# Kernel optimization log

Hardware: AMD Instinct MI355X
Metric: run time of the kernel (lower is better)

The kernel has to match this reference:

```python
import jax, jax.numpy as jnp
import numpy as np

STRIDES = [8, 16, 32, 64, 128]
SIZES = [32.0, 64.0, 128.0, 256.0, 512.0]
FEAT_HW = [(100, 152), (50, 76), (25, 38), (13, 19), (7, 10)]
N, C, A, K = 2, 256, 9, 80
SCORE_TH, TOPK, NMS_TH, MAX_DET = 0.05, 1000, 0.5, 100
IMG_H, IMG_W = 800.0, 1216.0
SCALE_CLAMP = float(np.log(1000.0 / 16.0))


def _cell_anchors(size):
    ratios = [0.5, 1.0, 2.0]
    scales = [2 ** 0, 2 ** (1.0 / 3), 2 ** (2.0 / 3)]
    out = []
    for s in scales:
        area = (size * s) ** 2
        for r in ratios:
            w = np.sqrt(area / r)
            h = w * r
            out.append([-w / 2.0, -h / 2.0, w / 2.0, h / 2.0])
    return np.asarray(out, np.float32)  # (9, 4)


def make_anchors():
    ancs = []
    for (H, W), st, sz in zip(FEAT_HW, STRIDES, SIZES):
        cell = _cell_anchors(sz)
        sx = np.arange(W, dtype=np.float32) * st
        sy = np.arange(H, dtype=np.float32) * st
        gx, gy = np.meshgrid(sx, sy)
        shifts = np.stack([gx.ravel(), gy.ravel(), gx.ravel(), gy.ravel()], 1)
        ancs.append((shifts[:, None, :] + cell[None, :, :]).reshape(-1, 4).astype(np.float32))
    return ancs


def setup_inputs() -> dict:
    key = jax.random.key(0)
    ks = jax.random.split(key, 10)
    inp = {}
    for i, (H, W) in enumerate(FEAT_HW):
        inp[f"feat{i}"] = jax.random.normal(ks[i], (N, C, H, W), jnp.float32)
    inp["cls_sub_w"] = jax.random.normal(ks[5], (4, C, C, 3, 3), jnp.float32) * 0.01
    inp["cls_sub_b"] = jnp.zeros((4, C), jnp.float32)
    inp["bbox_sub_w"] = jax.random.normal(ks[6], (4, C, C, 3, 3), jnp.float32) * 0.01
    inp["bbox_sub_b"] = jnp.zeros((4, C), jnp.float32)
    inp["cls_score_w"] = jax.random.normal(ks[7], (A * K, C, 3, 3), jnp.float32) * 0.1
    inp["cls_score_b"] = jnp.full((A * K,), float(-np.log((1 - 0.01) / 0.01)), jnp.float32)
    inp["bbox_pred_w"] = jax.random.normal(ks[8], (A * 4, C, 3, 3), jnp.float32) * 0.01
    inp["bbox_pred_b"] = jnp.zeros((A * 4,), jnp.float32)
    for i, a in enumerate(make_anchors()):
        inp[f"anc{i}"] = jnp.asarray(a)
    return inp


def conv3(x, w, b):
    y = jax.lax.conv_general_dilated(x, w, (1, 1), 'SAME',
                                     dimension_numbers=('NCHW', 'OIHW', 'NCHW'))
    return y + b[None, :, None, None]


def head_level(x, csw, csb, bsw, bsb, scw, scb, bpw, bpb):
    c = x
    r = x
    for i in range(4):
        c = jax.nn.relu(conv3(c, csw[i], csb[i]))
        r = jax.nn.relu(conv3(r, bsw[i], bsb[i]))
    return conv3(c, scw, scb), conv3(r, bpw, bpb)


def to_NHWA_K(t, k):
    n, _, h, w = t.shape
    return t.reshape(n, -1, k, h, w).transpose(0, 3, 4, 1, 2).reshape(n, -1, k)


def decode(deltas, anchors):
    wa = anchors[..., 2] - anchors[..., 0]
    ha = anchors[..., 3] - anchors[..., 1]
    xa = anchors[..., 0] + 0.5 * wa
    ya = anchors[..., 1] + 0.5 * ha
    dx, dy = deltas[..., 0], deltas[..., 1]
    dw = jnp.minimum(deltas[..., 2], SCALE_CLAMP)
    dh = jnp.minimum(deltas[..., 3], SCALE_CLAMP)
    cx = dx * wa + xa
    cy = dy * ha + ya
    w = jnp.exp(dw) * wa
    h = jnp.exp(dh) * ha
    return jnp.stack([cx - 0.5 * w, cy - 0.5 * h, cx + 0.5 * w, cy + 0.5 * h], -1)


def iou_vs_all(box, boxes):
    lt = jnp.maximum(box[:2], boxes[:, :2])
    rb = jnp.minimum(box[2:], boxes[:, 2:])
    wh = jnp.clip(rb - lt, 0.0)
    inter = wh[:, 0] * wh[:, 1]
    a1 = (box[2] - box[0]) * (box[3] - box[1])
    a2 = (boxes[:, 2] - boxes[:, 0]) * (boxes[:, 3] - boxes[:, 1])
    return inter / (a1 + a2 - inter + 1e-9)


def nms_image(boxes, scores, classes):
    # class-aware NMS via coordinate offset per class (batched_nms trick)
    off = classes.astype(boxes.dtype)[:, None] * 4096.0
    b = boxes + off

    def body(i, st):
        sc, bi, bs = st
        j = jnp.argmax(sc)
        s = sc[j]
        bi = bi.at[i].set(j)
        bs = bs.at[i].set(s)
        iou = iou_vs_all(b[j], b)
        sc = jnp.where(iou > NMS_TH, 0.0, sc).at[j].set(0.0)
        return (sc, bi, bs)

    bi0 = jnp.zeros((MAX_DET,), jnp.int32)
    bs0 = jnp.zeros((MAX_DET,), boxes.dtype)
    _, bi, bs = jax.lax.fori_loop(0, MAX_DET, body, (scores, bi0, bs0))
    return boxes[bi], bs, classes[bi]


def reference(feat0, feat1, feat2, feat3, feat4, cls_sub_w, cls_sub_b,
              bbox_sub_w, bbox_sub_b, cls_score_w, cls_score_b,
              bbox_pred_w, bbox_pred_b, anc0, anc1, anc2, anc3, anc4):
    feats = [feat0, feat1, feat2, feat3, feat4]
    ancs = [anc0, anc1, anc2, anc3, anc4]
    cand_b, cand_s, cand_c = [], [], []
    for f, anc in zip(feats, ancs):
        logits, deltas = head_level(f, cls_sub_w, cls_sub_b, bbox_sub_w, bbox_sub_b,
                                    cls_score_w, cls_score_b, bbox_pred_w, bbox_pred_b)
        cls = to_NHWA_K(logits, K)       # (N, HWA, K)
        reg = to_NHWA_K(deltas, 4)       # (N, HWA, 4)
        n, hwa, _ = reg.shape
        prob = jax.nn.sigmoid(cls.reshape(n, hwa * K))
        ntk = min(TOPK, hwa)             # d2: min(topk_candidates, box_reg_i.size(0))
        vals, idxs = jax.lax.top_k(prob, ntk)
        a_idx = idxs // K
        c_idx = idxs % K
        d = jnp.take_along_axis(reg, a_idx[..., None], axis=1)   # (N, ntk, 4)
        anc_sel = anc[a_idx]                                      # (N, ntk, 4)
        boxes = decode(d, anc_sel)
        boxes = jnp.stack([jnp.clip(boxes[..., 0], 0.0, IMG_W),
                           jnp.clip(boxes[..., 1], 0.0, IMG_H),
                           jnp.clip(boxes[..., 2], 0.0, IMG_W),
                           jnp.clip(boxes[..., 3], 0.0, IMG_H)], -1)
        scores = jnp.where(vals > SCORE_TH, vals, 0.0)  # score threshold (keep_idxs)
        cand_b.append(boxes)
        cand_s.append(scores)
        cand_c.append(c_idx)
    B = jnp.concatenate(cand_b, 1)
    S = jnp.concatenate(cand_s, 1)
    Cl = jnp.concatenate(cand_c, 1)
    det_boxes, det_scores, det_classes = jax.vmap(nms_image)(B, S, Cl)
    return det_boxes, det_scores, det_classes
```

## Files before the change

kernel.cpp:

```cpp
#include <hip/hip_runtime.h>
#include <math.h>

#define NIMG 2
#define NCAND 4630
#define MAXDET 100
#define IMG_W_F 1216.0f
#define IMG_H_F 800.0f
#define SCORE_THR 0.05f
#define NMS_THR 0.5f
#define SCALE_CLAMP_F 4.135166556742356f

typedef __attribute__((ext_vector_type(8))) _Float16 f16x8;
typedef __attribute__((ext_vector_type(16))) float f32x16;

#define WOFF_CLS_T(i) ((unsigned)(i) * 589824u)
#define WOFF_BBX_T(i) (2359296u + (unsigned)(i) * 589824u)
#define WOFF_CLS_H 4718592u
#define WOFF_BBX_H 6488064u

#define BUF_HALFS 10944000u
#define TK_SLOT_U32 139272

struct ConvTab {
  int cum[6];
  int H[5], W[5];
  unsigned actOff[5];
};
struct CvtTab {
  const float* f[5];
  int cumR[6];
  int H[5], W[5];
  unsigned actOff[5];
};
struct HeadTab {
  int cum[6];
  unsigned actOff[5];
  int H[5], W[5];
  int pOffL[5];
  int rOffL[5];
  int imgBase;
  int pImgStride;
};
struct TKTab {
  int pOff[9]; int M[9]; int kk[9]; int rBase[9]; int outBase[9];
  const float* anc[9];
};
struct PPTab {
  const float* src[10];
  unsigned dstOff[10];
  int Cout[10];
  int nCoF[10];
  int cum[11];
};

__global__ __launch_bounds__(256)
void prepack_k(_Float16* __restrict__ dst0, PPTab tb)
{
  int t0 = blockIdx.x * 256 + threadIdx.x;
  if (t0 >= tb.cum[10]) return;
  int r = 0;
  for (int i = 1; i < 10; ++i) if (t0 >= tb.cum[i]) r = i;
  const int t = t0 - tb.cum[r];
  const float* src = tb.src[r];
  _Float16* dst = dst0 + tb.dstOff[r];
  const int Cout = tb.Cout[r], nCoF = tb.nCoF[r];

  const int l = t & 63;
  const int rest = t >> 6;
  const int coF = rest % nCoF;
  const int tc = rest / nCoF;
  const int tap = tc >> 4;
  const int cb = tc & 15;
  const int co = coF * 32 + (l & 31);
  const int ciB = cb * 16 + (l >> 5) * 8;
#pragma unroll
  for (int j = 0; j < 8; ++j) {
    float v = 0.f;
    if (co < Cout) v = src[(size_t)(co * 256 + ciB + j) * 9 + tap];
    dst[(size_t)t * 8 + j] = (_Float16)v;
  }
}

__global__ __launch_bounds__(256)
void convert_k(_Float16* __restrict__ act, CvtTab tb)
{
  int bz = blockIdx.x;
  int l = 0;
#pragma unroll
  for (int i = 1; i < 5; ++i) if (bz >= tb.cumR[i]) l = i;
  const int h = bz - tb.cumR[l];
  const int n = blockIdx.y;
  const int H = tb.H[l], W = tb.W[l];
  const int Hp = H + 2, Wp = W + 2, HpWp = Hp * Wp;
  const unsigned CBS = 2u * (unsigned)HpWp * 16u;
  const float* x = tb.f[l];
  _Float16* a = act + tb.actOff[l];
  __shared__ float s[64][154];
  for (int c0 = 0; c0 < 256; c0 += 64) {
    for (int idx = threadIdx.x; idx < 64 * W; idx += 256) {
      int c = idx / W, w = idx - c * W;
      s[c][w] = x[((size_t)(n * 256 + c0 + c) * H + h) * W + w];
    }
    __syncthreads();
    for (int idx = threadIdx.x; idx < 4 * W; idx += 256) {
      int ch = idx / W, w = idx - ch * W;
      int cchunk = (c0 >> 4) + ch;
      unsigned base = (unsigned)cchunk * CBS +
                      ((unsigned)((n * Hp + h + 1) * Wp + (w + 1))) * 16u;
      f16x8 v0, v1;
#pragma unroll
      for (int j = 0; j < 8; ++j) {
        v0[j] = (_Float16)s[ch * 16 + j][w];
        v1[j] = (_Float16)s[ch * 16 + 8 + j][w];
      }
      *(f16x8*)(a + base) = v0;
      *(f16x8*)(a + base + 8) = v1;
    }
    __syncthreads();
  }
}

__device__ __forceinline__ void conv_core(
    const _Float16* __restrict__ in, const _Float16* __restrict__ w,
    int nCoF, int coF0, int Wp, unsigned CBS, const unsigned V0, const unsigned V1,
    unsigned lOff, f32x16& a00, f32x16& a01, f32x16& a10, f32x16& a11)
{
  for (int cb = 0; cb < 16; ++cb) {
    const _Float16* aB = in + (unsigned)cb * CBS;
    const _Float16* wB = w + ((unsigned)cb * (unsigned)nCoF + (unsigned)coF0) * 512u;
#pragma unroll
    for (int tap = 0; tap < 9; ++tap) {
      const unsigned to = ((unsigned)((tap / 3) * Wp + (tap % 3))) * 16u;
      const _Float16* wT = wB + (unsigned)tap * 16u * (unsigned)nCoF * 512u;
      f16x8 a0 = *(const f16x8*)(aB + to + V0);
      f16x8 a1 = *(const f16x8*)(aB + to + V1);
      f16x8 b0 = *(const f16x8*)(wT + lOff);
      f16x8 b1 = *(const f16x8*)(wT + 512u + lOff);
      a00 = __builtin_amdgcn_mfma_f32_32x32x16_f16(a0, b0, a00, 0, 0, 0);
      a01 = __builtin_amdgcn_mfma_f32_32x32x16_f16(a0, b1, a01, 0, 0, 0);
      a10 = __builtin_amdgcn_mfma_f32_32x32x16_f16(a1, b0, a10, 0, 0, 0);
      a11 = __builtin_amdgcn_mfma_f32_32x32x16_f16(a1, b1, a11, 0, 0, 0);
    }
  }
}

__global__ __launch_bounds__(256)
void tower_k(const _Float16* __restrict__ inA, const _Float16* __restrict__ inB,
             const _Float16* __restrict__ wpk,
             const float* __restrict__ biasA, const float* __restrict__ biasB,
             _Float16* __restrict__ outA, _Float16* __restrict__ outB,
             unsigned wOffA, unsigned wOffB, ConvTab tb)
{
  int bz = blockIdx.x;
  int l = 0;
#pragma unroll
  for (int i = 1; i < 5; ++i) if (bz >= tb.cum[i]) l = i;
  const int bx = bz - tb.cum[l];
  const int H = tb.H[l], W = tb.W[l];
  const int Wp = W + 2, HW = H * W, HpWp = (H + 2) * Wp;
  const unsigned CBS = 2u * (unsigned)HpWp * 16u;
  const int chain = blockIdx.y >> 2, cg = blockIdx.y & 3;
  const _Float16* in = (chain ? inB : inA) + tb.actOff[l];
  _Float16* out = (chain ? outB : outA) + tb.actOff[l];
  const _Float16* w = wpk + (chain ? wOffB : wOffA);
  const float* bias = chain ? biasB : biasA;
  const int Mloc = 2 * HW;

  const int wave = threadIdx.x >> 6;
  const int lane = threadIdx.x & 63;
  const int lw = lane & 31;
  const int lh = lane >> 5;
  const int mBase = bx * 256 + wave * 64;
  unsigned V[2];
#pragma unroll
  for (int i = 0; i < 2; ++i) {
    int mloc = mBase + i * 32 + lw;
    if (mloc >= Mloc) mloc = Mloc - 1;
    int n = mloc / HW; int rem = mloc - n * HW;
    int h = rem / W; int ww = rem - h * W;
    V[i] = ((unsigned)(n * HpWp + h * Wp + ww)) * 16u + (unsigned)lh * 8u;
  }
  f32x16 a00 = {}, a01 = {}, a10 = {}, a11 = {};
  conv_core(in, w, 8, cg * 2, Wp, CBS, V[0], V[1], (unsigned)lane * 8u,
            a00, a01, a10, a11);

  const int coBase = cg * 64;
  const f32x16* accs[4] = {&a00, &a01, &a10, &a11};
#pragma unroll
  for (int q = 0; q < 4; ++q) {
    const f32x16& A = *accs[q];
    const int i = q >> 1, f = q & 1;
    const int co = coBase + f * 32 + lw;
    const float bv = bias[co];
#pragma unroll
    for (int r = 0; r < 16; ++r) {
      int mloc = mBase + i * 32 + ((r & 3) + 8 * (r >> 2) + 4 * lh);
      if (mloc >= Mloc) continue;
      int n = mloc / HW; int rem = mloc - n * HW;
      int h = rem / W; int ww = rem - h * W;
      unsigned addr = ((unsigned)(co >> 4)) * CBS +
                      ((unsigned)(n * HpWp + (h + 1) * Wp + (ww + 1))) * 16u +
                      (unsigned)(co & 15);
      out[addr] = (_Float16)fmaxf(A[r] + bv, 0.f);
    }
  }
}

__global__ __launch_bounds__(256)
void head_k(const _Float16* __restrict__ inC, const _Float16* __restrict__ inX,
            const _Float16* __restrict__ wpk,
            const float* __restrict__ scb, const float* __restrict__ bpb,
            float* __restrict__ P, _Float16* __restrict__ Rh, HeadTab tb)
{
  int bz = blockIdx.y;
  int li = 0;
#pragma unroll
  for (int i = 1; i < 5; ++i) if (bz >= tb.cum[i]) li = i;
  const int bx = bz - tb.cum[li];
  const int H = tb.H[li], W = tb.W[li];
  const int Wp = W + 2, HW = H * W, HpWp = (H + 2) * Wp;
  const unsigned CBS = 2u * (unsigned)HpWp * 16u;
  const int img = tb.imgBase + blockIdx.z;
  const int y = blockIdx.x;

  const _Float16* in;
  const _Float16* w;
  const float* bias;
  int nCoF, coF0, coBase, Cout;
  if (y < 12) {
    in = inC + tb.actOff[li]; w = wpk + WOFF_CLS_H; bias = scb;
    nCoF = 24; coF0 = y * 2; coBase = y * 64; Cout = 720;
  } else {
    in = inX + tb.actOff[li]; w = wpk + WOFF_BBX_H; bias = bpb;
    nCoF = 2; coF0 = 0; coBase = 0; Cout = 36;
  }
  const int Mloc = HW;
  const int wave = threadIdx.x >> 6;
  const int lane = threadIdx.x & 63;
  const int lw = lane & 31;
  const int lh = lane >> 5;
  const int mBase = bx * 256 + wave * 64;
  unsigned V[2];
#pragma unroll
  for (int i = 0; i < 2; ++i) {
    int mloc = mBase + i * 32 + lw;
    if (mloc >= Mloc) mloc = Mloc - 1;
    int h = mloc / W; int ww = mloc - h * W;
    V[i] = ((unsigned)(img * HpWp + h * Wp + ww)) * 16u + (unsigned)lh * 8u;
  }
  f32x16 a00 = {}, a01 = {}, a10 = {}, a11 = {};
  conv_core(in, w, nCoF, coF0, Wp, CBS, V[0], V[1], (unsigned)lane * 8u,
            a00, a01, a10, a11);

  const size_t pBase = (size_t)tb.pOffL[li] + (size_t)blockIdx.z * tb.pImgStride;
  const size_t rBase = (size_t)tb.rOffL[li] + (size_t)img * HW * 36;
  const f32x16* accs[4] = {&a00, &a01, &a10, &a11};
#pragma unroll
  for (int q = 0; q < 4; ++q) {
    const f32x16& A = *accs[q];
    const int i = q >> 1, f = q & 1;
    const int co = coBase + f * 32 + lw;
    const float bv = (co < Cout) ? bias[co] : 0.f;
#pragma unroll
    for (int r = 0; r < 16; ++r) {
      int mloc = mBase + i * 32 + ((r & 3) + 8 * (r >> 2) + 4 * lh);
      if (mloc >= Mloc) continue;
      float v = A[r] + bv;
      if (y < 12) {
        if (co < 720) P[pBase + (size_t)mloc * 720 + co] = 1.f / (1.f + expf(-v));
      } else {
        if (co < 36) Rh[rBase + (size_t)mloc * 36 + co] = (_Float16)v;
      }
    }
  }
}

__global__ __launch_bounds__(256)
void hist_coarse_k(const float* __restrict__ wsF, unsigned* __restrict__ tkbuf, TKTab t)
{
  const int slot = blockIdx.y;
  __shared__ unsigned lh[8192];
  for (int i = threadIdx.x; i < 8192; i += 256) lh[i] = 0;
  __syncthreads();
  const float* p = wsF + t.pOff[slot];
  const int M = t.M[slot];
  for (int i = blockIdx.x * 256 + threadIdx.x; i < M; i += gridDim.x * 256)
    atomicAdd(&lh[(__float_as_uint(p[i]) >> 17) & 8191u], 1u);
  __syncthreads();
  unsigned* h = tkbuf + (size_t)slot * TK_SLOT_U32;
  for (int i = threadIdx.x; i < 8192; i += 256) {
    unsigned c = lh[i];
    if (c) atomicAdd(&h[i], c);
  }
}

__global__ __launch_bounds__(256)
void hist_fine_k(const float* __restrict__ wsF, unsigned* __restrict__ tkbuf, TKTab t)
{
  const int slot = blockIdx.y;
  unsigned* base = tkbuf + (size_t)slot * TK_SLOT_U32;
  const unsigned cb = base[8192 + 131072 + 0];
  const float* p = wsF + t.pOff[slot];
  const int M = t.M[slot];
  unsigned* h = base + 8192;
  for (int i = blockIdx.x * 256 + threadIdx.x; i < M; i += gridDim.x * 256) {
    unsigned b = __float_as_uint(p[i]);
    if ((b >> 17) == cb) atomicAdd(&h[b & 0x1FFFFu], 1u);
  }
}

__global__ __launch_bounds__(1024)
void radix_scan_k(unsigned* __restrict__ tkbuf, TKTab t, int phase)
{
  const int slot = blockIdx.x;
  unsigned* base = tkbuf + (size_t)slot * TK_SLOT_U32;
  const unsigned* hb0 = base + (phase ? 8192 : 0);
  unsigned* s = base + 8192 + 131072;
  const int nbins = phase ? 131072 : 8192;
  const int k = t.kk[slot];
  const int per = nbins / 1024;
  const int tid = threadIdx.x;
  const unsigned* hb = hb0 + tid * per;
  unsigned local = 0;
  for (int i = 0; i < per; ++i) local += hb[i];
  __shared__ unsigned part[1024];
  part[tid] = local;
  __syncthreads();
  for (int d = 1; d < 1024; d <<= 1) {
    unsigned v = (tid + d < 1024) ? part[tid + d] : 0u;
    __syncthreads();
    part[tid] += v;
    __syncthreads();
  }
  unsigned above = part[tid] - local;
  unsigned kk = (phase == 0) ? (unsigned)k : ((unsigned)k - s[1]);
  if (above < kk && above + local >= kk) {
    unsigned cum = above;
    for (int i = per - 1; i >= 0; --i) {
      unsigned c = hb[i];
      if (cum + c >= kk) {
        if (phase == 0) { s[0] = (unsigned)(tid * per + i); s[1] = cum; }
        else { s[2] = (s[0] << 17) | (unsigned)(tid * per + i); s[4] = kk - cum; }
        break;
      }
      cum += c;
    }
  }
}

__global__ __launch_bounds__(256)
void compact_k(const float* __restrict__ wsF, unsigned* __restrict__ tkbuf,
               float* __restrict__ cv, unsigned* __restrict__ ci,
               unsigned* __restrict__ eq, TKTab t)
{
  const int slot = blockIdx.y;
  unsigned* s = tkbuf + (size_t)slot * TK_SLOT_U32 + 8192 + 131072;
  const unsigned thr = s[2];
  const float* p = wsF + t.pOff[slot];
  const int M = t.M[slot];
  float* cvn = cv + slot * 1024;
  unsigned* cin_ = ci + slot * 1024;
  unsigned* eqn = eq + (size_t)slot * 8192;
  for (int i = blockIdx.x * 256 + threadIdx.x; i < M; i += gridDim.x * 256) {
    unsigned b = __float_as_uint(p[i]);
    if (b > thr) {
      unsigned g = atomicAdd(&s[5], 1u);
      if (g < 1024u) { cvn[g] = p[i]; cin_[g] = (unsigned)i; }
    } else if (b == thr) {
      unsigned e = atomicAdd(&s[6], 1u);
      if (e < 8192u) eqn[e] = (unsigned)i;
    }
  }
}

__global__ __launch_bounds__(1024)
void finalize_k(const float* __restrict__ cv, const unsigned* __restrict__ ci,
                const unsigned* __restrict__ eq, const unsigned* __restrict__ tkbuf,
                const _Float16* __restrict__ Rh, TKTab t,
                float* __restrict__ candB, float* __restrict__ candS, float* __restrict__ candC)
{
  const int slot = blockIdx.x;
  const int tid = threadIdx.x;
  const unsigned* s = tkbuf + (size_t)slot * TK_SLOT_U32 + 8192 + 131072;
  const float* anc = t.anc[slot];
  const int k = t.kk[slot];
  __shared__ float svals[1024];
  __shared__ unsigned sidx[1024];
  __shared__ unsigned long long key[1024];
  const unsigned cntG = s[5] < 1024u ? s[5] : 1024u;
  const unsigned nEq = s[4];
  if (tid < (int)cntG) {
    svals[tid] = cv[slot * 1024 + tid];
    sidx[tid] = ci[slot * 1024 + tid];
  }
  __syncthreads();
  if (tid == 0) {
    unsigned cnt = s[6] < 8192u ? s[6] : 8192u;
    unsigned last = 0; int first = 1;
    float tv = __uint_as_float(s[2]);
    for (unsigned e2 = 0; e2 < nEq && cntG + e2 < 1024u; ++e2) {
      unsigned best = 0xFFFFFFFFu;
      for (unsigned q = 0; q < cnt; ++q) {
        unsigned v = eq[(size_t)slot * 8192 + q];
        if ((first || v > last) && v < best) best = v;
      }
      svals[cntG + e2] = tv; sidx[cntG + e2] = best;
      last = best; first = 0;
    }
  }
  __syncthreads();
  const int kk = (int)cntG + (int)nEq;
  key[tid] = (tid < kk)
      ? (((unsigned long long)__float_as_uint(svals[tid]) << 32) |
         (unsigned long long)(0xFFFFFFFFu - sidx[tid]))
      : 0ULL;
  __syncthreads();
  for (int sz = 2; sz <= 1024; sz <<= 1) {
    for (int st = sz >> 1; st > 0; st >>= 1) {
      int ixj = tid ^ st;
      if (ixj > tid) {
        unsigned long long a = key[tid], b = key[ixj];
        bool up = ((tid & sz) == 0);
        if (up ? (a < b) : (a > b)) { key[tid] = b; key[ixj] = a; }
      }
      __syncthreads();
    }
  }
  if (tid < kk && tid < k) {
    unsigned long long kv = key[tid];
    float val = __uint_as_float((unsigned)(kv >> 32));
    unsigned idx = 0xFFFFFFFFu - (unsigned)(kv & 0xFFFFFFFFu);
    unsigned a = idx / 80u;
    unsigned cls = idx - a * 80u;
    const _Float16* rg = Rh + (size_t)t.rBase[slot] + (size_t)a * 4;
    float a0 = anc[(size_t)a * 4 + 0], a1 = anc[(size_t)a * 4 + 1];
    float a2 = anc[(size_t)a * 4 + 2], a3 = anc[(size_t)a * 4 + 3];
    float wa = a2 - a0, ha = a3 - a1;
    float xa = a0 + 0.5f * wa, ya = a1 + 0.5f * ha;
    float dx = (float)rg[0], dy = (float)rg[1];
    float dw = fminf((float)rg[2], SCALE_CLAMP_F), dh = fminf((float)rg[3], SCALE_CLAMP_F);
    float cx = dx * wa + xa, cy = dy * ha + ya;
    float wb = expf(dw) * wa, hb = expf(dh) * ha;
    float x0 = cx - 0.5f * wb, y0 = cy - 0.5f * hb;
    float x1 = cx + 0.5f * wb, y1 = cy + 0.5f * hb;
    x0 = fminf(fmaxf(x0, 0.f), IMG_W_F);
    y0 = fminf(fmaxf(y0, 0.f), IMG_H_F);
    x1 = fminf(fmaxf(x1, 0.f), IMG_W_F);
    y1 = fminf(fmaxf(y1, 0.f), IMG_H_F);
    int o = t.outBase[slot] + tid;
    candB[(size_t)o * 4 + 0] = x0; candB[(size_t)o * 4 + 1] = y0;
    candB[(size_t)o * 4 + 2] = x1; candB[(size_t)o * 4 + 3] = y1;
    candS[o] = (val > SCORE_THR) ? val : 0.f;
    candC[o] = (float)cls;
  }
}

__global__ __launch_bounds__(1024)
void nms_k(const float* __restrict__ cB, const float* __restrict__ cS,
           const float* __restrict__ cC, float* __restrict__ out)
{
  const int n = blockIdx.x;
  const int tid = threadIdx.x;
  const int wid = tid >> 6, lane = tid & 63;
  __shared__ float S[NCAND];
  __shared__ float wv_[16];
  __shared__ int wi_[16];
  __shared__ float bj[5];
  __shared__ int sjs;
  for (int i = tid; i < NCAND; i += 1024) S[i] = cS[n * NCAND + i];
  __syncthreads();
  for (int it = 0; it < MAXDET; ++it) {
    float bv = -1.f; int bix = 0;
    for (int i = tid; i < NCAND; i += 1024) {
      float v = S[i];
      if (v > bv) { bv = v; bix = i; }
    }
#pragma unroll
    for (int d = 32; d > 0; d >>= 1) {
      float v2 = __shfl_down(bv, d);
      int i2 = __shfl_down(bix, d);
      if (v2 > bv || (v2 == bv && i2 < bix)) { bv = v2; bix = i2; }
    }
    if (lane == 0) { wv_[wid] = bv; wi_[wid] = bix; }
    __syncthreads();
    if (tid < 64) {
      float v = (tid < 16) ? wv_[tid] : -2.f;
      int ix = (tid < 16) ? wi_[tid] : 0x7FFFFFFF;
#pragma unroll
      for (int d = 8; d > 0; d >>= 1) {
        float v2 = __shfl_down(v, d);
        int i2 = __shfl_down(ix, d);
        if (v2 > v || (v2 == v && i2 < ix)) { v = v2; ix = i2; }
      }
      if (tid == 0) {
        bj[4] = v; sjs = ix;
        if (v > 0.f) {
          const int j = ix;
          float b0 = cB[(size_t)(n * NCAND + j) * 4 + 0];
          float b1 = cB[(size_t)(n * NCAND + j) * 4 + 1];
          float b2 = cB[(size_t)(n * NCAND + j) * 4 + 2];
          float b3 = cB[(size_t)(n * NCAND + j) * 4 + 3];
          out[((size_t)n * MAXDET + it) * 4 + 0] = b0;
          out[((size_t)n * MAXDET + it) * 4 + 1] = b1;
          out[((size_t)n * MAXDET + it) * 4 + 2] = b2;
          out[((size_t)n * MAXDET + it) * 4 + 3] = b3;
          out[800 + n * MAXDET + it] = v;
          out[1000 + n * MAXDET + it] = cC[n * NCAND + j];
          float off = cC[n * NCAND + j] * 4096.f;
          bj[0] = b0 + off; bj[1] = b1 + off; bj[2] = b2 + off; bj[3] = b3 + off;
        }
      }
    }
    __syncthreads();
    const float mv = bj[4];
    const int j = sjs;
    if (mv <= 0.f) {
      float b0 = cB[(size_t)(n * NCAND) * 4 + 0], b1 = cB[(size_t)(n * NCAND) * 4 + 1];
      float b2 = cB[(size_t)(n * NCAND) * 4 + 2], b3 = cB[(size_t)(n * NCAND) * 4 + 3];
      float c0 = cC[n * NCAND];
      for (int t2 = it + tid; t2 < MAXDET; t2 += 1024) {
        out[((size_t)n * MAXDET + t2) * 4 + 0] = b0;
        out[((size_t)n * MAXDET + t2) * 4 + 1] = b1;
        out[((size_t)n * MAXDET + t2) * 4 + 2] = b2;
        out[((size_t)n * MAXDET + t2) * 4 + 3] = b3;
        out[800 + n * MAXDET + t2] = 0.f;
        out[1000 + n * MAXDET + t2] = c0;
      }
      return;
    }
    const float jx0 = bj[0], jy0 = bj[1], jx1 = bj[2], jy1 = bj[3];
    const float aj = (jx1 - jx0) * (jy1 - jy0);
    for (int i = tid; i < NCAND; i += 1024) {
      if (i == j) { S[i] = 0.f; continue; }
      if (S[i] == 0.f) continue;
      float off = cC[n * NCAND + i] * 4096.f;
      float x0 = cB[(size_t)(n * NCAND + i) * 4 + 0] + off;
      float y0 = cB[(size_t)(n * NCAND + i) * 4 + 1] + off;
      float x1 = cB[(size_t)(n * NCAND + i) * 4 + 2] + off;
      float y1 = cB[(size_t)(n * NCAND + i) * 4 + 3] + off;
      float lx = fmaxf(jx0, x0), ly = fmaxf(jy0, y0);
      float rx = fminf(jx1, x1), ry = fminf(jy1, y1);
      float iw = fmaxf(rx - lx, 0.f), ih = fmaxf(ry - ly, 0.f);
      float inter = iw * ih;
      float ai = (x1 - x0) * (y1 - y0);
      float iou = inter / (aj + ai - inter + 1e-9f);
      if (iou > NMS_THR) S[i] = 0.f;
    }
    __syncthreads();
  }
}

extern "C" void kernel_launch(void* const* d_in, const int* in_sizes, int n_in,
                              void* d_out, int out_size, void* d_ws, size_t ws_size,
                              hipStream_t stream)
{
  static const int LH[5] = {100, 50, 25, 13, 7};
  static const int LW[5] = {152, 76, 38, 19, 10};
  static const int LHW[5] = {15200, 3800, 950, 247, 70};
  static const int NTK[5] = {1000, 1000, 1000, 1000, 630};
  static const int OFFS[5] = {0, 1000, 2000, 3000, 4000};
  static const unsigned ACTOFF[5] = {0u, 8042496u, 10119168u, 10672128u, 10833408u};
  static const int CUMT[6] = {0, 119, 149, 157, 159, 160};
  static const int CUMR[6] = {0, 100, 150, 175, 188, 195};
  static const int ROFF[5] = {0, 1094400, 1368000, 1436400, 1454184};
  static const int POFF14[4] = {0, 2736000, 3420000, 3597840};
  static const int PSTRIDE14 = 3648240;

  const float* feat[5]; const float* anc[5];
  for (int l = 0; l < 5; ++l) {
    feat[l] = (const float*)d_in[l];
    anc[l] = (const float*)d_in[13 + l];
  }
  const float* csw = (const float*)d_in[5];
  const float* csb = (const float*)d_in[6];
  const float* bsw = (const float*)d_in[7];
  const float* bsb = (const float*)d_in[8];
  const float* scw = (const float*)d_in[9];
  const float* scb = (const float*)d_in[10];
  const float* bpw = (const float*)d_in[11];
  const float* bpb = (const float*)d_in[12];

  float* wsF = (float*)d_ws;
  size_t o = 0;
  _Float16* actBase = (_Float16*)(wsF + o); o += (size_t)4 * BUF_HALFS / 2;
  _Float16* wpk = (_Float16*)(wsF + o); o += 3317760;
  float* P0 = wsF + o; o += 10944000;
  _Float16* Rh = (_Float16*)(wsF + o); o += 729612;
  float* candB = wsF + o; o += (size_t)NIMG * NCAND * 4;
  float* candS = wsF + o; o += NIMG * NCAND;
  float* candC = wsF + o; o += NIMG * NCAND;
  float* candV = wsF + o; o += 9 * 1024;
  unsigned* candI = (unsigned*)(wsF + o); o += 9 * 1024;
  unsigned* eqI = (unsigned*)(wsF + o); o += 9 * 8192;
  unsigned* tkbuf = (unsigned*)(wsF + o); o += (size_t)9 * TK_SLOT_U32;
  if (ws_size < o * sizeof(float)) return;

  _Float16* X = actBase;
  _Float16* A = X + BUF_HALFS;
  _Float16* B = A + BUF_HALFS;
  _Float16* C = B + BUF_HALFS;
  float* P1 = (float*)A;
  float* out = (float*)d_out;

  {
    PPTab pp;
    static const int PPC[11] = {0, 73728, 147456, 221184, 294912, 368640,
                                442368, 516096, 589824, 811008, 829440};
    for (int i = 0; i < 11; ++i) pp.cum[i] = PPC[i];
    for (int i = 0; i < 4; ++i) {
      pp.src[i] = csw + (size_t)i * 589824; pp.dstOff[i] = WOFF_CLS_T(i);
      pp.Cout[i] = 256; pp.nCoF[i] = 8;
      pp.src[4 + i] = bsw + (size_t)i * 589824; pp.dstOff[4 + i] = WOFF_BBX_T(i);
      pp.Cout[4 + i] = 256; pp.nCoF[4 + i] = 8;
    }
    pp.src[8] = scw; pp.dstOff[8] = WOFF_CLS_H; pp.Cout[8] = 720; pp.nCoF[8] = 24;
    pp.src[9] = bpw; pp.dstOff[9] = WOFF_BBX_H; pp.Cout[9] = 36; pp.nCoF[9] = 2;
    prepack_k<<<dim3(3240), dim3(256), 0, stream>>>(wpk, pp);
  }

  hipMemsetAsync(actBase, 0, (size_t)4 * BUF_HALFS * 2, stream);

  ConvTab ct;
  CvtTab vt;
  for (int l = 0; l < 5; ++l) {
    ct.H[l] = LH[l]; ct.W[l] = LW[l]; ct.actOff[l] = ACTOFF[l];
    vt.f[l] = feat[l]; vt.H[l] = LH[l]; vt.W[l] = LW[l]; vt.actOff[l] = ACTOFF[l];
  }
  for (int i = 0; i < 6; ++i) { ct.cum[i] = CUMT[i]; vt.cumR[i] = CUMR[i]; }

  convert_k<<<dim3(195, NIMG), dim3(256), 0, stream>>>(X, vt);

  tower_k<<<dim3(160, 8), dim3(256), 0, stream>>>(X, X, wpk, csb + 0, bsb + 0, A, B,
      WOFF_CLS_T(0), WOFF_BBX_T(0), ct);
  tower_k<<<dim3(160, 8), dim3(256), 0, stream>>>(A, B, wpk, csb + 256, bsb + 256, C, X,
      WOFF_CLS_T(1), WOFF_BBX_T(1), ct);
  tower_k<<<dim3(160, 8), dim3(256), 0, stream>>>(C, X, wpk, csb + 512, bsb + 512, A, B,
      WOFF_CLS_T(2), WOFF_BBX_T(2), ct);
  tower_k<<<dim3(160, 8), dim3(256), 0, stream>>>(A, B, wpk, csb + 768, bsb + 768, C, X,
      WOFF_CLS_T(3), WOFF_BBX_T(3), ct);

  auto runTopk = [&](const TKTab& tk, int nslot) {
    hipMemsetAsync(tkbuf, 0, (size_t)nslot * TK_SLOT_U32 * 4, stream);
    hist_coarse_k<<<dim3(256, nslot), dim3(256), 0, stream>>>(wsF, tkbuf, tk);
    radix_scan_k<<<dim3(nslot), dim3(1024), 0, stream>>>(tkbuf, tk, 0);
    hist_fine_k<<<dim3(256, nslot), dim3(256), 0, stream>>>(wsF, tkbuf, tk);
    radix_scan_k<<<dim3(nslot), dim3(1024), 0, stream>>>(tkbuf, tk, 1);
    compact_k<<<dim3(256, nslot), dim3(256), 0, stream>>>(wsF, tkbuf, candV, candI, eqI, tk);
    finalize_k<<<dim3(nslot), dim3(1024), 0, stream>>>(candV, candI, eqI, tkbuf, Rh, tk,
                                                       candB, candS, candC);
  };

  const int p0Off = (int)(P0 - wsF);
  const int p1Off = (int)(P1 - wsF);

  {
    HeadTab ht = {};
    ht.cum[0] = 0; ht.cum[1] = 60;
    for (int i = 2; i < 6; ++i) ht.cum[i] = 0x7FFFFFFF;
    ht.actOff[0] = ACTOFF[0]; ht.H[0] = LH[0]; ht.W[0] = LW[0];
    ht.pOffL[0] = 0; ht.rOffL[0] = ROFF[0];
    ht.imgBase = 0; ht.pImgStride = 0;
    head_k<<<dim3(13, 60, 1), dim3(256), 0, stream>>>(C, X, wpk, scb, bpb, P0, Rh, ht);
    TKTab tk = {};
    tk.pOff[0] = p0Off; tk.M[0] = LHW[0] * 720; tk.kk[0] = NTK[0];
    tk.rBase[0] = ROFF[0];
    tk.outBase[0] = OFFS[0];
    tk.anc[0] = anc[0];
    runTopk(tk, 1);
  }
  {
    HeadTab ht = {};
    ht.cum[0] = 0; ht.cum[1] = 60;
    for (int i = 2; i < 6; ++i) ht.cum[i] = 0x7FFFFFFF;
    ht.actOff[0] = ACTOFF[0]; ht.H[0] = LH[0]; ht.W[0] = LW[0];
    ht.pOffL[0] = 0; ht.rOffL[0] = ROFF[0];
    ht.imgBase = 1; ht.pImgStride = 0;
    head_k<<<dim3(13, 60, 1), dim3(256), 0, stream>>>(C, X, wpk, scb, bpb, P1, Rh, ht);
  }
  {
    HeadTab ht = {};
    static const int CUMH14[6] = {0, 15, 19, 20, 21, 0x7FFFFFFF};
    for (int i = 0; i < 6; ++i) ht.cum[i] = CUMH14[i];
    for (int i = 0; i < 4; ++i) {
      int l = i + 1;
      ht.actOff[i] = ACTOFF[l]; ht.H[i] = LH[l]; ht.W[i] = LW[l];
      ht.pOffL[i] = POFF14[i]; ht.rOffL[i] = ROFF[l];
    }
    ht.imgBase = 0; ht.pImgStride = PSTRIDE14;
    head_k<<<dim3(13, 21, 2), dim3(256), 0, stream>>>(C, X, wpk, scb, bpb, P0, Rh, ht);
    TKTab tk = {};
    tk.pOff[0] = p1Off; tk.M[0] = LHW[0] * 720; tk.kk[0] = NTK[0];
    tk.rBase[0] = ROFF[0] + LHW[0] * 36;
    tk.outBase[0] = NCAND + OFFS[0];
    tk.anc[0] = anc[0];
    for (int s = 1; s < 9; ++s) {
      int i = s - 1;
      int l = (i & 3) + 1, img = i >> 2;
      tk.pOff[s] = p0Off + img * PSTRIDE14 + POFF14[l - 1];
      tk.M[s] = LHW[l] * 720;
      tk.kk[s] = NTK[l];
      tk.rBase[s] = ROFF[l] + img * LHW[l] * 36;
      tk.outBase[s] = img * NCAND + OFFS[l];
      tk.anc[s] = anc[l];
    }
    runTopk(tk, 9);
  }
  nms_k<<<dim3(NIMG), dim3(1024), 0, stream>>>(candB, candS, candC, out);
}
```

Baseline: 1.619 ms.

## Widen conv output tiles to 128 channels and zero only halo borders

Result: slower. 2.455 ms (+51.6%).

```diff
diff --git a/kernel.cpp b/kernel.cpp
--- a/kernel.cpp
+++ b/kernel.cpp
@@ -52,6 +52,11 @@
   int nCoF[10];
   int cum[11];
 };
+struct HaloTab {
+  int cumPx[6];
+  int Hp[5], Wp[5];
+  unsigned actOff[5];
+};
 
 __global__ __launch_bounds__(256)
 void prepack_k(_Float16* __restrict__ dst0, PPTab tb)
@@ -79,6 +84,33 @@
     if (co < Cout) v = src[(size_t)(co * 256 + ciB + j) * 9 + tap];
     dst[(size_t)t * 8 + j] = (_Float16)v;
   }
+}
+
+__global__ __launch_bounds__(256)
+void halo_k(_Float16* __restrict__ actBase, HaloTab tb)
+{
+  int t = blockIdx.x * 256 + threadIdx.x;
+  if (t >= 4 * 16 * 2 * 1000) return;
+  const int buf = t / 32000;
+  int r = t - buf * 32000;
+  const int cbimg = r / 1000;
+  const int px = r - cbimg * 1000;
+  const int cb = cbimg >> 1, img = cbimg & 1;
+  int l = 0;
+#pragma unroll
+  for (int i = 1; i < 5; ++i) if (px >= tb.cumPx[i]) l = i;
+  const int pxl = px - tb.cumPx[l];
+  const int Hp = tb.Hp[l], Wp = tb.Wp[l];
+  int hp, wp;
+  if (pxl < Wp) { hp = 0; wp = pxl; }
+  else if (pxl < 2 * Wp) { hp = Hp - 1; wp = pxl - Wp; }
+  else { int q = pxl - 2 * Wp; hp = 1 + (q >> 1); wp = (q & 1) ? (Wp - 1) : 0; }
+  const unsigned CBS = 2u * (unsigned)(Hp * Wp) * 16u;
+  _Float16* a = actBase + (size_t)buf * BUF_HALFS + tb.actOff[l] +
+                (unsigned)cb * CBS + ((unsigned)((img * Hp + hp) * Wp + wp)) * 16u;
+  f16x8 z = {};
+  *(f16x8*)(a) = z;
+  *(f16x8*)(a + 8) = z;
 }
 
 __global__ __launch_bounds__(256)
@@ -120,26 +152,31 @@
   }
 }
 
-__device__ __forceinline__ void conv_core(
+template<int NF>
+__device__ __forceinline__ void conv_coreN(
     const _Float16* __restrict__ in, const _Float16* __restrict__ w,
     int nCoF, int coF0, int Wp, unsigned CBS, const unsigned V0, const unsigned V1,
-    unsigned lOff, f32x16& a00, f32x16& a01, f32x16& a10, f32x16& a11)
-{
+    unsigned lOff, f32x16* __restrict__ acc)
+{
+  const unsigned wTap = 16u * (unsigned)nCoF * 512u;
   for (int cb = 0; cb < 16; ++cb) {
     const _Float16* aB = in + (unsigned)cb * CBS;
     const _Float16* wB = w + ((unsigned)cb * (unsigned)nCoF + (unsigned)coF0) * 512u;
 #pragma unroll
     for (int tap = 0; tap < 9; ++tap) {
       const unsigned to = ((unsigned)((tap / 3) * Wp + (tap % 3))) * 16u;
-      const _Float16* wT = wB + (unsigned)tap * 16u * (unsigned)nCoF * 512u;
+      const _Float16* wT = wB + (unsigned)tap * wTap;
       f16x8 a0 = *(const f16x8*)(aB + to + V0);
       f16x8 a1 = *(const f16x8*)(aB + to + V1);
-      f16x8 b0 = *(const f16x8*)(wT + lOff);
-      f16x8 b1 = *(const f16x8*)(wT + 512u + lOff);
-      a00 = __builtin_amdgcn_mfma_f32_32x32x16_f16(a0, b0, a00, 0, 0, 0);
-      a01 = __builtin_amdgcn_mfma_f32_32x32x16_f16(a0, b1, a01, 0, 0, 0);
-      a10 = __builtin_amdgcn_mfma_f32_32x32x16_f16(a1, b0, a10, 0, 0, 0);
-      a11 = __builtin_amdgcn_mfma_f32_32x32x16_f16(a1, b1, a11, 0, 0, 0);
+      f16x8 b[NF];
+#pragma unroll
+      for (int f = 0; f < NF; ++f)
+        b[f] = *(const f16x8*)(wT + (unsigned)f * 512u + lOff);
+#pragma unroll
+      for (int f = 0; f < NF; ++f) {
+        acc[2 * f + 0] = __builtin_amdgcn_mfma_f32_32x32x16_f16(a0, b[f], acc[2 * f + 0], 0, 0, 0);
+        acc[2 * f + 1] = __builtin_amdgcn_mfma_f32_32x32x16_f16(a1, b[f], acc[2 * f + 1], 0, 0, 0);
+      }
     }
   }
 }
@@ -151,7 +188,7 @@
              _Float16* __restrict__ outA, _Float16* __restrict__ outB,
              unsigned wOffA, unsigned wOffB, ConvTab tb)
 {
-  int bz = blockIdx.x;
+  int bz = blockIdx.y;
   int l = 0;
 #pragma unroll
   for (int i = 1; i < 5; ++i) if (bz >= tb.cum[i]) l = i;
@@ -159,7 +196,7 @@
   const int H = tb.H[l], W = tb.W[l];
   const int Wp = W + 2, HW = H * W, HpWp = (H + 2) * Wp;
   const unsigned CBS = 2u * (unsigned)HpWp * 16u;
-  const int chain = blockIdx.y >> 2, cg = blockIdx.y & 3;
+  const int chain = blockIdx.x >> 1, cg2 = blockIdx.x & 1;
   const _Float16* in = (chain ? inB : inA) + tb.actOff[l];
   _Float16* out = (chain ? outB : outA) + tb.actOff[l];
   const _Float16* w = wpk + (chain ? wOffB : wOffA);
@@ -180,28 +217,28 @@
     int h = rem / W; int ww = rem - h * W;
     V[i] = ((unsigned)(n * HpWp + h * Wp + ww)) * 16u + (unsigned)lh * 8u;
   }
-  f32x16 a00 = {}, a01 = {}, a10 = {}, a11 = {};
-  conv_core(in, w, 8, cg * 2, Wp, CBS, V[0], V[1], (unsigned)lane * 8u,
-            a00, a01, a10, a11);
-
-  const int coBase = cg * 64;
-  const f32x16* accs[4] = {&a00, &a01, &a10, &a11};
-#pragma unroll
-  for (int q = 0; q < 4; ++q) {
-    const f32x16& A = *accs[q];
-    const int i = q >> 1, f = q & 1;
-    const int co = coBase + f * 32 + lw;
-    const float bv = bias[co];
-#pragma unroll
-    for (int r = 0; r < 16; ++r) {
-      int mloc = mBase + i * 32 + ((r & 3) + 8 * (r >> 2) + 4 * lh);
-      if (mloc >= Mloc) continue;
-      int n = mloc / HW; int rem = mloc - n * HW;
-      int h = rem / W; int ww = rem - h * W;
-      unsigned addr = ((unsigned)(co >> 4)) * CBS +
-                      ((unsigned)(n * HpWp + (h + 1) * Wp + (ww + 1))) * 16u +
-                      (unsigned)(co & 15);
-      out[addr] = (_Float16)fmaxf(A[r] + bv, 0.f);
+  f32x16 acc[8] = {};
+  conv_coreN<4>(in, w, 8, cg2 * 4, Wp, CBS, V[0], V[1], (unsigned)lane * 8u, acc);
+
+  const int coBase = cg2 * 128;
+#pragma unroll
+  for (int f = 0; f < 4; ++f) {
+#pragma unroll
+    for (int i = 0; i < 2; ++i) {
+      const f32x16& A = acc[2 * f + i];
+      const int co = coBase + f * 32 + lw;
+      const float bv = bias[co];
+#pragma unroll
+      for (int r = 0; r < 16; ++r) {
+        int mloc = mBase + i * 32 + ((r & 3) + 8 * (r >> 2) + 4 * lh);
+        if (mloc >= Mloc) continue;
+        int n = mloc / HW; int rem = mloc - n * HW;
+        int h = rem / W; int ww = rem - h * W;
+        unsigned addr = ((unsigned)(co >> 4)) * CBS +
+                        ((unsigned)(n * HpWp + (h + 1) * Wp + (ww + 1))) * 16u +
+                        (unsigned)(co & 15);
+        out[addr] = (_Float16)fmaxf(A[r] + bv, 0.f);
+      }
     }
   }
 }
@@ -223,17 +260,6 @@
   const int img = tb.imgBase + blockIdx.z;
   const int y = blockIdx.x;
 
-  const _Float16* in;
-  const _Float16* w;
-  const float* bias;
-  int nCoF, coF0, coBase, Cout;
-  if (y < 12) {
-    in = inC + tb.actOff[li]; w = wpk + WOFF_CLS_H; bias = scb;
-    nCoF = 24; coF0 = y * 2; coBase = y * 64; Cout = 720;
-  } else {
-    in = inX + tb.actOff[li]; w = wpk + WOFF_BBX_H; bias = bpb;
-    nCoF = 2; coF0 = 0; coBase = 0; Cout = 36;
-  }
   const int Mloc = HW;
   const int wave = threadIdx.x >> 6;
   const int lane = threadIdx.x & 63;
@@ -248,28 +274,48 @@
     int h = mloc / W; int ww = mloc - h * W;
     V[i] = ((unsigned)(img * HpWp + h * Wp + ww)) * 16u + (unsigned)lh * 8u;
   }
-  f32x16 a00 = {}, a01 = {}, a10 = {}, a11 = {};
-  conv_core(in, w, nCoF, coF0, Wp, CBS, V[0], V[1], (unsigned)lane * 8u,
-            a00, a01, a10, a11);
-
   const size_t pBase = (size_t)tb.pOffL[li] + (size_t)blockIdx.z * tb.pImgStride;
   const size_t rBase = (size_t)tb.rOffL[li] + (size_t)img * HW * 36;
-  const f32x16* accs[4] = {&a00, &a01, &a10, &a11};
-#pragma unroll
-  for (int q = 0; q < 4; ++q) {
-    const f32x16& A = *accs[q];
-    const int i = q >> 1, f = q & 1;
-    const int co = coBase + f * 32 + lw;
-    const float bv = (co < Cout) ? bias[co] : 0.f;
-#pragma unroll
-    for (int r = 0; r < 16; ++r) {
-      int mloc = mBase + i * 32 + ((r & 3) + 8 * (r >> 2) + 4 * lh);
-      if (mloc >= Mloc) continue;
-      float v = A[r] + bv;
-      if (y < 12) {
-        if (co < 720) P[pBase + (size_t)mloc * 720 + co] = 1.f / (1.f + expf(-v));
-      } else {
-        if (co < 36) Rh[rBase + (size_t)mloc * 36 + co] = (_Float16)v;
+
+  if (y < 6) {
+    const _Float16* in = inC + tb.actOff[li];
+    f32x16 acc[8] = {};
+    conv_coreN<4>(in, wpk + WOFF_CLS_H, 24, y * 4, Wp, CBS, V[0], V[1],
+                  (unsigned)lane * 8u, acc);
+    const int coBase = y * 128;
+#pragma unroll
+    for (int f = 0; f < 4; ++f) {
+#pragma unroll
+      for (int i = 0; i < 2; ++i) {
+        const f32x16& A = acc[2 * f + i];
+        const int co = coBase + f * 32 + lw;
+        const float bv = (co < 720) ? scb[co] : 0.f;
+#pragma unroll
+        for (int r = 0; r < 16; ++r) {
+          int mloc = mBase + i * 32 + ((r & 3) + 8 * (r >> 2) + 4 * lh);
+          if (mloc >= Mloc || co >= 720) continue;
+          P[pBase + (size_t)mloc * 720 + co] = 1.f / (1.f + expf(-(A[r] + bv)));
+        }
+      }
+    }
+  } else {
+    const _Float16* in = inX + tb.actOff[li];
+    f32x16 acc[4] = {};
+    conv_coreN<2>(in, wpk + WOFF_BBX_H, 2, 0, Wp, CBS, V[0], V[1],
+                  (unsigned)lane * 8u, acc);
+#pragma unroll
+    for (int f = 0; f < 2; ++f) {
+#pragma unroll
+      for (int i = 0; i < 2; ++i) {
+        const f32x16& A = acc[2 * f + i];
+        const int co = f * 32 + lw;
+        const float bv = (co < 36) ? bpb[co] : 0.f;
+#pragma unroll
+        for (int r = 0; r < 16; ++r) {
+          int mloc = mBase + i * 32 + ((r & 3) + 8 * (r >> 2) + 4 * lh);
+          if (mloc >= Mloc || co >= 36) continue;
+          Rh[rBase + (size_t)mloc * 36 + co] = (_Float16)(A[r] + bv);
+        }
       }
     }
   }
@@ -618,7 +664,15 @@
     prepack_k<<<dim3(3240), dim3(256), 0, stream>>>(wpk, pp);
   }
 
-  hipMemsetAsync(actBase, 0, (size_t)4 * BUF_HALFS * 2, stream);
+  {
+    HaloTab hzt;
+    static const int HCUM[6] = {0, 508, 764, 894, 962, 1000};
+    for (int i = 0; i < 6; ++i) hzt.cumPx[i] = HCUM[i];
+    for (int l = 0; l < 5; ++l) {
+      hzt.Hp[l] = LH[l] + 2; hzt.Wp[l] = LW[l] + 2; hzt.actOff[l] = ACTOFF[l];
+    }
+    halo_k<<<dim3((128000 + 255) / 256), dim3(256), 0, stream>>>(X, hzt);
+  }
 
   ConvTab ct;
   CvtTab vt;
@@ -630,13 +684,13 @@
 
   convert_k<<<dim3(195, NIMG), dim3(256), 0, stream>>>(X, vt);
 
-  tower_k<<<dim3(160, 8), dim3(256), 0, stream>>>(X, X, wpk, csb + 0, bsb + 0, A, B,
+  tower_k<<<dim3(4, 160), dim3(256), 0, stream>>>(X, X, wpk, csb + 0, bsb + 0, A, B,
       WOFF_CLS_T(0), WOFF_BBX_T(0), ct);
-  tower_k<<<dim3(160, 8), dim3(256), 0, stream>>>(A, B, wpk, csb + 256, bsb + 256, C, X,
+  tower_k<<<dim3(4, 160), dim3(256), 0, stream>>>(A, B, wpk, csb + 256, bsb + 256, C, X,
       WOFF_CLS_T(1), WOFF_BBX_T(1), ct);
-  tower_k<<<dim3(160, 8), dim3(256), 0, stream>>>(C, X, wpk, csb + 512, bsb + 512, A, B,
+  tower_k<<<dim3(4, 160), dim3(256), 0, stream>>>(C, X, wpk, csb + 512, bsb + 512, A, B,
       WOFF_CLS_T(2), WOFF_BBX_T(2), ct);
-  tower_k<<<dim3(160, 8), dim3(256), 0, stream>>>(A, B, wpk, csb + 768, bsb + 768, C, X,
+  tower_k<<<dim3(4, 160), dim3(256), 0, stream>>>(A, B, wpk, csb + 768, bsb + 768, C, X,
       WOFF_CLS_T(3), WOFF_BBX_T(3), ct);
 
   auto runTopk = [&](const TKTab& tk, int nslot) {
@@ -660,7 +714,7 @@
     ht.actOff[0] = ACTOFF[0]; ht.H[0] = LH[0]; ht.W[0] = LW[0];
     ht.pOffL[0] = 0; ht.rOffL[0] = ROFF[0];
     ht.imgBase = 0; ht.pImgStride = 0;
-    head_k<<<dim3(13, 60, 1), dim3(256), 0, stream>>>(C, X, wpk, scb, bpb, P0, Rh, ht);
+    head_k<<<dim3(7, 60, 1), dim3(256), 0, stream>>>(C, X, wpk, scb, bpb, P0, Rh, ht);
     TKTab tk = {};
     tk.pOff[0] = p0Off; tk.M[0] = LHW[0] * 720; tk.kk[0] = NTK[0];
     tk.rBase[0] = ROFF[0];
@@ -675,7 +729,7 @@
     ht.actOff[0] = ACTOFF[0]; ht.H[0] = LH[0]; ht.W[0] = LW[0];
     ht.pOffL[0] = 0; ht.rOffL[0] = ROFF[0];
     ht.imgBase = 1; ht.pImgStride = 0;
-    head_k<<<dim3(13, 60, 1), dim3(256), 0, stream>>>(C, X, wpk, scb, bpb, P1, Rh, ht);
+    head_k<<<dim3(7, 60, 1), dim3(256), 0, stream>>>(C, X, wpk, scb, bpb, P1, Rh, ht);
   }
   {
     HeadTab ht = {};
@@ -687,7 +741,7 @@
       ht.pOffL[i] = POFF14[i]; ht.rOffL[i] = ROFF[l];
     }
     ht.imgBase = 0; ht.pImgStride = PSTRIDE14;
-    head_k<<<dim3(13, 21, 2), dim3(256), 0, stream>>>(C, X, wpk, scb, bpb, P0, Rh, ht);
+    head_k<<<dim3(7, 21, 2), dim3(256), 0, stream>>>(C, X, wpk, scb, bpb, P0, Rh, ht);
     TKTab tk = {};
     tk.pOff[0] = p1Off; tk.M[0] = LHW[0] * 720; tk.kk[0] = NTK[0];
     tk.rBase[0] = ROFF[0] + LHW[0] * 36;
```
